# Performance work log

Hardware: AMD Instinct MI355X
Metric: run time of the kernel (lower is better)

The kernel has to match this reference:

```python
import jax, jax.numpy as jnp
import numpy as np

N_NODES = 100000


def _gcn_conv(x, row, col, W, b, n):
    # PyG GCNConv: h = W x; out_i = sum_{j->i} norm_ij * h_j + b, with self-loops
    # and symmetric normalization norm_ij = deg_i^-1/2 * deg_j^-1/2.
    h = x @ W  # [N, out]
    loop = jnp.arange(n, dtype=row.dtype)
    r = jnp.concatenate([row, loop])
    c = jnp.concatenate([col, loop])
    deg = jax.ops.segment_sum(jnp.ones_like(c, dtype=h.dtype), c, num_segments=n)
    dinv = jnp.where(deg > 0, jax.lax.rsqrt(deg), 0.0)
    norm = dinv[r] * dinv[c]  # [E+N]
    msg = h[r] * norm[:, None]  # gather + per-edge scale
    out = jax.ops.segment_sum(msg, c, num_segments=n)  # scatter-add to dst
    return out + b


def setup_inputs() -> dict:
    key = jax.random.key(0)
    ks = jax.random.split(key, 8)
    N, E = N_NODES, 1600000
    d_in, comm_dim, hid, out = 120, 8, 128, 64
    x = jax.random.normal(ks[0], (N, d_in), dtype=jnp.float32)
    edge_index = jax.random.randint(ks[1], (2, E), 0, N, dtype=jnp.int64)
    comm_ids = jax.random.randint(ks[2], (N,), 0, 64, dtype=jnp.int64)
    comm_emb = jax.random.normal(ks[3], (64, comm_dim), dtype=jnp.float32)
    s1 = 1.0 / np.sqrt(d_in + comm_dim)
    s2 = 1.0 / np.sqrt(hid)
    W1 = jax.random.normal(ks[4], (d_in + comm_dim, hid), dtype=jnp.float32) * s1
    b1 = jnp.zeros((hid,), dtype=jnp.float32)
    W2 = jax.random.normal(ks[5], (hid, out), dtype=jnp.float32) * s2
    b2 = jnp.zeros((out,), dtype=jnp.float32)
    return {"x": x, "edge_index": edge_index, "comm_ids": comm_ids,
            "comm_emb": comm_emb, "W1": W1, "b1": b1, "W2": W2, "b2": b2}


def reference(x, edge_index, comm_ids, comm_emb, W1, b1, W2, b2):
    n = x.shape[0]
    row, col = edge_index[0], edge_index[1]
    c = comm_emb[comm_ids]                      # [N, comm_dim] embedding lookup
    h = jnp.concatenate([x, c], axis=-1)        # [N, in+comm_dim]
    h = jax.nn.relu(_gcn_conv(h, row, col, W1, b1, n))
    # dropout p=0.5 is inactive in eval mode (training=False)
    out = _gcn_conv(h, row, col, W2, b2, n)     # [N, out_channels]
    return out
```

## Files before the change

kernel.cpp:

```cpp
#include <hip/hip_runtime.h>

typedef __attribute__((ext_vector_type(8))) short bf16x8;
typedef __attribute__((ext_vector_type(4))) float f32x4;

#define CAPB 5632
#define NBMAX 512

static __device__ __forceinline__ unsigned short f2bf(float f) {
    unsigned u = __float_as_uint(f);
    unsigned r = (u + 0x7fff + ((u >> 16) & 1)) >> 16;
    return (unsigned short)r;
}
static __device__ __forceinline__ float bfu_lo(unsigned v) { return __uint_as_float(v << 16); }
static __device__ __forceinline__ float bfu_hi(unsigned v) { return __uint_as_float(v & 0xffff0000u); }
static __device__ __forceinline__ unsigned packbf(float a, float b) {
    return (unsigned)f2bf(a) | ((unsigned)f2bf(b) << 16);
}

static __device__ __forceinline__ bf16x8 cvt8(float4 u0, float4 u1) {
    bf16x8 r;
    r[0] = (short)f2bf(u0.x); r[1] = (short)f2bf(u0.y);
    r[2] = (short)f2bf(u0.z); r[3] = (short)f2bf(u0.w);
    r[4] = (short)f2bf(u1.x); r[5] = (short)f2bf(u1.y);
    r[6] = (short)f2bf(u1.z); r[7] = (short)f2bf(u1.w);
    return r;
}

__global__ void k_zero_int(int* __restrict__ p, int n) {
    int i = blockIdx.x * blockDim.x + threadIdx.x;
    if (i < n) p[i] = 0;
}

__global__ __launch_bounds__(256) void k_passA(const int* __restrict__ row,
                                               const int* __restrict__ col,
                                               int* __restrict__ gcnt,
                                               unsigned* __restrict__ packed,
                                               int E, int NB) {
    __shared__ int lcnt[NBMAX];
    __shared__ int lbase[NBMAX];
    __shared__ int lcur[NBMAX];
    __shared__ int gbaseS[NBMAX];
    __shared__ unsigned stage[4096];
    __shared__ unsigned short stageb[4096];
    __shared__ int s[256];

    int tid = threadIdx.x;
    int t0 = blockIdx.x * 4096;
    int total = min(4096, E - t0);

    for (int b = tid; b < NBMAX; b += 256) { lcnt[b] = 0; lcur[b] = 0; }
    __syncthreads();

    int er[16], ec[16];
#pragma unroll
    for (int j = 0; j < 16; ++j) {
        int e = t0 + j * 256 + tid;
        if (e < E) {
            er[j] = row[e];
            ec[j] = col[e];
            atomicAdd(&lcnt[ec[j] >> 8], 1);
        }
    }
    __syncthreads();

    int c0 = lcnt[2 * tid], c1 = lcnt[2 * tid + 1];
    int p = c0 + c1;
    s[tid] = p;
    __syncthreads();
    for (int off = 1; off < 256; off <<= 1) {
        int t = (tid >= off) ? s[tid - off] : 0;
        __syncthreads();
        s[tid] += t;
        __syncthreads();
    }
    int ebase = s[tid] - p;
    lbase[2 * tid] = ebase;
    lbase[2 * tid + 1] = ebase + c0;
    __syncthreads();

    for (int b = tid; b < NB; b += 256) {
        int lc = lcnt[b];
        if (lc > 0) gbaseS[b] = atomicAdd(&gcnt[b], lc);
    }
    __syncthreads();

#pragma unroll
    for (int j = 0; j < 16; ++j) {
        int e = t0 + j * 256 + tid;
        if (e < E) {
            int b = ec[j] >> 8;
            int pos = lbase[b] + atomicAdd(&lcur[b], 1);
            stage[pos] = ((unsigned)er[j] << 8) | ((unsigned)ec[j] & 255u);
            stageb[pos] = (unsigned short)b;
        }
    }
    __syncthreads();

    for (int j = tid; j < total; j += 256) {
        int b = stageb[j];
        packed[(size_t)b * CAPB + gbaseS[b] + (j - lbase[b])] = stage[j];
    }
}

__global__ void k_bscan(const int* __restrict__ gcnt, int* __restrict__ gbase,
                        int* __restrict__ indptr, int n, int E, int NB) {
    __shared__ int s[512];
    int tid = threadIdx.x;
    int v = (tid < NB) ? gcnt[tid] : 0;
    s[tid] = v;
    __syncthreads();
    for (int off = 1; off < 512; off <<= 1) {
        int t = (tid >= off) ? s[tid - off] : 0;
        __syncthreads();
        s[tid] += t;
        __syncthreads();
    }
    if (tid < NB) gbase[tid] = s[tid] - v;
    if (tid == 0) indptr[n] = E;
}

__global__ __launch_bounds__(256) void k_passB(const unsigned* __restrict__ packed,
                                               const int* __restrict__ gcnt,
                                               const int* __restrict__ gbase,
                                               int* __restrict__ indptr,
                                               float* __restrict__ dinv,
                                               int* __restrict__ srcidx, int n) {
    __shared__ int ncnt[256];
    __shared__ int nbase[256];
    __shared__ int srow[CAPB];

    int b = blockIdx.x;
    int tid = threadIdx.x;
    int nodeBase = b << 8;
    int cntE = min(gcnt[b], CAPB);
    int base = gbase[b];
    size_t pb = (size_t)b * CAPB;

    ncnt[tid] = 0;
    __syncthreads();

    for (int j = tid; j < cntE; j += 256) {
        unsigned e = packed[pb + j];
        atomicAdd(&ncnt[e & 255u], 1);
    }
    __syncthreads();

    int v = ncnt[tid];
    nbase[tid] = v;
    __syncthreads();
    for (int off = 1; off < 256; off <<= 1) {
        int t = (tid >= off) ? nbase[tid - off] : 0;
        __syncthreads();
        nbase[tid] += t;
        __syncthreads();
    }
    int excl = nbase[tid] - v;
    __syncthreads();
    nbase[tid] = excl;

    int node = nodeBase + tid;
    if (node < n) {
        indptr[node] = base + excl;
        dinv[node] = rsqrtf((float)(v + 1));
    }
    ncnt[tid] = 0;
    __syncthreads();

    for (int j = tid; j < cntE; j += 256) {
        unsigned e = packed[pb + j];
        int c = (int)(e & 255u);
        int r = (int)(e >> 8);
        int p = nbase[c] + atomicAdd(&ncnt[c], 1);
        srow[p] = r;
    }
    __syncthreads();

    for (int j = tid; j < cntE; j += 256) srcidx[base + j] = srow[j];
}

__global__ void k_wprep(const float* __restrict__ W1, const float* __restrict__ W2,
                        unsigned short* __restrict__ Wt1, unsigned short* __restrict__ Wt2p) {
    int idx = blockIdx.x * blockDim.x + threadIdx.x;
    if (idx < 128 * 128) {
        int colc = idx >> 7, k = idx & 127;
        Wt1[colc * 128 + k] = f2bf(W1[k * 128 + colc]);
    } else if (idx < 128 * 128 + 64 * 128) {
        int j = idx - 128 * 128;
        int colc = j >> 7, p = j & 127;
        int korig = (p & 7) * 16 + (p >> 3);
        Wt2p[colc * 128 + p] = f2bf(W2[korig * 64 + colc]);
    }
}

__global__ __launch_bounds__(256) void k_gemm1(const float* __restrict__ x,
                                               const int* __restrict__ cid,
                                               const float* __restrict__ cemb,
                                               const unsigned short* __restrict__ Wt,
                                               const float* __restrict__ dinv,
                                               unsigned char* __restrict__ D1q,
                                               float* __restrict__ scales, int n) {
    int tid = threadIdx.x;
    int wid = tid >> 6, lane = tid & 63;
    int rbase = blockIdx.x * 64 + wid * 16;
    int lr = lane & 15, kq = lane >> 4;

    int arow = rbase + lr;
    if (arow > n - 1) arow = n - 1;
    const float* xp = x + (size_t)arow * 120 + kq * 8;

    bf16x8 a0 = cvt8(*(const float4*)(xp),      *(const float4*)(xp + 4));
    bf16x8 a1 = cvt8(*(const float4*)(xp + 32), *(const float4*)(xp + 36));
    bf16x8 a2 = cvt8(*(const float4*)(xp + 64), *(const float4*)(xp + 68));
    bf16x8 a3;
    if (kq < 3) {
        a3 = cvt8(*(const float4*)(xp + 96), *(const float4*)(xp + 100));
    } else {
        const float* cp = cemb + (size_t)cid[arow] * 8;
        a3 = cvt8(*(const float4*)(cp), *(const float4*)(cp + 4));
    }

    f32x4 acc[8];
#pragma unroll
    for (int cf = 0; cf < 8; ++cf) acc[cf] = (f32x4){0.f, 0.f, 0.f, 0.f};

#pragma unroll
    for (int cf = 0; cf < 8; ++cf) {
        const unsigned short* bp = Wt + (size_t)(cf * 16 + lr) * 128 + kq * 8;
        bf16x8 b0 = *(const bf16x8*)(bp);
        bf16x8 b1 = *(const bf16x8*)(bp + 32);
        bf16x8 b2 = *(const bf16x8*)(bp + 64);
        bf16x8 b3 = *(const bf16x8*)(bp + 96);
        acc[cf] = __builtin_amdgcn_mfma_f32_16x16x32_bf16(a0, b0, acc[cf], 0, 0, 0);
        acc[cf] = __builtin_amdgcn_mfma_f32_16x16x32_bf16(a1, b1, acc[cf], 0, 0, 0);
        acc[cf] = __builtin_amdgcn_mfma_f32_16x16x32_bf16(a2, b2, acc[cf], 0, 0, 0);
        acc[cf] = __builtin_amdgcn_mfma_f32_16x16x32_bf16(a3, b3, acc[cf], 0, 0, 0);
    }

#pragma unroll
    for (int r = 0; r < 4; ++r) {
        int grow = rbase + kq * 4 + r;
        float dv = (grow < n) ? dinv[grow] : 0.f;
        float m = 0.f;
#pragma unroll
        for (int cf = 0; cf < 8; ++cf) m = fmaxf(m, fabsf(acc[cf][r] * dv));
        m = fmaxf(m, __shfl_xor(m, 1));
        m = fmaxf(m, __shfl_xor(m, 2));
        m = fmaxf(m, __shfl_xor(m, 4));
        m = fmaxf(m, __shfl_xor(m, 8));
        float sinv = (m > 1e-20f) ? 127.f / m : 0.f;
        if (grow < n) {
            if (lr == 0) scales[grow] = m * (1.f / 127.f);
            unsigned lo = 0, hi = 0;
#pragma unroll
            for (int cf = 0; cf < 4; ++cf) {
                int q8 = (int)rintf(acc[cf][r] * dv * sinv);
                lo |= ((unsigned)(q8 & 255)) << (8 * cf);
            }
#pragma unroll
            for (int cf = 4; cf < 8; ++cf) {
                int q8 = (int)rintf(acc[cf][r] * dv * sinv);
                hi |= ((unsigned)(q8 & 255)) << (8 * (cf - 4));
            }
            *(uint2*)&D1q[(size_t)grow * 128 + lr * 8] = make_uint2(lo, hi);
        }
    }
}

template <int NOUT>
__global__ __launch_bounds__(256) void k_gemm_bf16(const unsigned short* __restrict__ A,
                                                   const unsigned short* __restrict__ Wt,
                                                   const float* __restrict__ dinv,
                                                   unsigned short* __restrict__ D, int n) {
    constexpr int NCF = NOUT / 16;
    int tid = threadIdx.x;
    int wid = tid >> 6, lane = tid & 63;
    int rbase = blockIdx.x * 64 + wid * 16;
    int lr = lane & 15, kq = lane >> 4;

    int arow = rbase + lr;
    if (arow > n - 1) arow = n - 1;
    const unsigned short* ap = A + (size_t)arow * 128 + kq * 8;
    bf16x8 a0 = *(const bf16x8*)(ap);
    bf16x8 a1 = *(const bf16x8*)(ap + 32);
    bf16x8 a2 = *(const bf16x8*)(ap + 64);
    bf16x8 a3 = *(const bf16x8*)(ap + 96);

    f32x4 acc[NCF];
#pragma unroll
    for (int cf = 0; cf < NCF; ++cf) acc[cf] = (f32x4){0.f, 0.f, 0.f, 0.f};

#pragma unroll
    for (int cf = 0; cf < NCF; ++cf) {
        const unsigned short* bp = Wt + (size_t)(cf * 16 + lr) * 128 + kq * 8;
        bf16x8 b0 = *(const bf16x8*)(bp);
        bf16x8 b1 = *(const bf16x8*)(bp + 32);
        bf16x8 b2 = *(const bf16x8*)(bp + 64);
        bf16x8 b3 = *(const bf16x8*)(bp + 96);
        acc[cf] = __builtin_amdgcn_mfma_f32_16x16x32_bf16(a0, b0, acc[cf], 0, 0, 0);
        acc[cf] = __builtin_amdgcn_mfma_f32_16x16x32_bf16(a1, b1, acc[cf], 0, 0, 0);
        acc[cf] = __builtin_amdgcn_mfma_f32_16x16x32_bf16(a2, b2, acc[cf], 0, 0, 0);
        acc[cf] = __builtin_amdgcn_mfma_f32_16x16x32_bf16(a3, b3, acc[cf], 0, 0, 0);
    }

    float dv[4];
#pragma unroll
    for (int r = 0; r < 4; ++r) {
        int grow = rbase + kq * 4 + r;
        dv[r] = (grow < n) ? dinv[grow] : 0.f;
    }
#pragma unroll
    for (int cf = 0; cf < NCF; ++cf) {
#pragma unroll
        for (int r = 0; r < 4; ++r) {
            int grow = rbase + kq * 4 + r;
            if (grow < n) D[(size_t)grow * NOUT + cf * 16 + lr] = f2bf(acc[cf][r] * dv[r]);
        }
    }
}

__global__ __launch_bounds__(64) void k_agg1(const unsigned char* __restrict__ Hq,
                                             const float* __restrict__ scales,
                                             const int* __restrict__ indptr,
                                             const int* __restrict__ srcidx,
                                             const float* __restrict__ dinv,
                                             const float* __restrict__ bias,
                                             unsigned* __restrict__ Out, int n) {
    int i = blockIdx.x;
    int lane = threadIdx.x;
    int c0 = ((2 * lane) & 7) * 16 + (lane >> 2);
    float bx = bias[c0], by = bias[c0 + 16];
    float di = dinv[i];

    unsigned short sq = *(const unsigned short*)(Hq + (size_t)i * 128 + 2 * lane);
    float ss = scales[i];
    float ax = ss * (float)(signed char)(sq & 255);
    float ay = ss * (float)(signed char)(sq >> 8);

    int e0 = indptr[i], e1 = indptr[i + 1];
#pragma unroll 4
    for (int e = e0; e < e1; ++e) {
        int s = srcidx[e];
        unsigned short q = *(const unsigned short*)(Hq + (size_t)s * 128 + 2 * lane);
        float sc = scales[s];
        ax += sc * (float)(signed char)(q & 255);
        ay += sc * (float)(signed char)(q >> 8);
    }
    float ox = fmaxf(di * ax + bx, 0.f);
    float oy = fmaxf(di * ay + by, 0.f);
    Out[(size_t)i * 64 + lane] = packbf(ox, oy);
}

__global__ __launch_bounds__(64) void k_agg2(const unsigned* __restrict__ Hs,
                                             const int* __restrict__ indptr,
                                             const int* __restrict__ srcidx,
                                             const float* __restrict__ dinv,
                                             const float* __restrict__ bias,
                                             float2* __restrict__ Out, int n) {
    int i = blockIdx.x;
    int lane = threadIdx.x;
    int v = lane & 31, h = lane >> 5;
    float di = dinv[i];
    float2 b = *(const float2*)&bias[v * 2];
    float ax = 0.f, ay = 0.f;
    if (h == 0) {
        unsigned sv = Hs[(size_t)i * 32 + v];
        ax = bfu_lo(sv);
        ay = bfu_hi(sv);
    }
    int e0 = indptr[i], e1 = indptr[i + 1];
#pragma unroll 4
    for (int e = e0 + h; e < e1; e += 2) {
        unsigned w = Hs[(size_t)srcidx[e] * 32 + v];
        ax += bfu_lo(w);
        ay += bfu_hi(w);
    }
    ax += __shfl_xor(ax, 32);
    ay += __shfl_xor(ay, 32);
    if (h == 0) {
        Out[(size_t)i * 32 + v] = make_float2(di * ax + b.x, di * ay + b.y);
    }
}


extern "C" void kernel_launch(void* const* d_in, const int* in_sizes, int n_in,
                              void* d_out, int out_size, void* d_ws, size_t ws_size,
                              hipStream_t stream) {
    const float* x    = (const float*)d_in[0];
    const int*   eidx = (const int*)d_in[1];
    const int*   cid  = (const int*)d_in[2];
    const float* cemb = (const float*)d_in[3];
    const float* W1   = (const float*)d_in[4];
    const float* b1   = (const float*)d_in[5];
    const float* W2   = (const float*)d_in[6];
    const float* b2   = (const float*)d_in[7];
    float* out = (float*)d_out;

    int n = in_sizes[2];
    int E = in_sizes[1] / 2;
    const int* row = eidx;
    const int* col = eidx + E;
    int NB = (n + 255) / 256;

    char* ws = (char*)d_ws;
    auto alloc = [&](size_t bytes) {
        char* p = ws;
        ws += (bytes + 255) & ~(size_t)255;
        return p;
    };
    float*          dinv   = (float*)alloc((size_t)n * 4);
    int*            gcnt   = (int*)alloc((size_t)NB * 4);
    int*            gbase  = (int*)alloc((size_t)NB * 4);
    int*            indptr = (int*)alloc((size_t)(n + 1) * 4);
    int*            srcidx = (int*)alloc((size_t)E * 4);
    unsigned*       packed = (unsigned*)alloc((size_t)NB * CAPB * 4);
    unsigned short* Wt1    = (unsigned short*)alloc(128 * 128 * 2);
    unsigned short* Wt2p   = (unsigned short*)alloc(64 * 128 * 2);
    unsigned char*  D1q    = (unsigned char*)alloc((size_t)n * 128);
    float*          scales = (float*)alloc((size_t)n * 4);
    unsigned short* H1p    = (unsigned short*)alloc((size_t)n * 128 * 2);
    unsigned short* D2     = (unsigned short*)alloc((size_t)n * 64 * 2);

    k_zero_int<<<(NB + 255) / 256, 256, 0, stream>>>(gcnt, NB);
    k_passA<<<(E + 4095) / 4096, 256, 0, stream>>>(row, col, gcnt, packed, E, NB);
    k_bscan<<<1, 512, 0, stream>>>(gcnt, gbase, indptr, n, E, NB);
    k_passB<<<NB, 256, 0, stream>>>(packed, gcnt, gbase, indptr, dinv, srcidx, n);

    k_wprep<<<(128 * 128 + 64 * 128 + 255) / 256, 256, 0, stream>>>(W1, W2, Wt1, Wt2p);

    int gb = (n + 63) / 64;
    k_gemm1<<<gb, 256, 0, stream>>>(x, cid, cemb, Wt1, dinv, D1q, scales, n);
    k_agg1<<<n, 64, 0, stream>>>(D1q, scales, indptr, srcidx, dinv, b1,
                                 (unsigned*)H1p, n);
    k_gemm_bf16<64><<<gb, 256, 0, stream>>>(H1p, Wt2p, dinv, D2, n);
    k_agg2<<<n, 64, 0, stream>>>((const unsigned*)D2, indptr, srcidx, dinv, b2,
                                 (float2*)out, n);
}
```

Baseline: 213.2 us.

## Pack four nodes per wavefront in aggregation kernels with wider per-lane loads

Both aggregation kernels now map four destination nodes onto each 64-lane wavefront, 16 lanes per node, instead of one node per block. Each lane loads 8 bytes per neighbor row (8 int8 or 4 bf16 values) rather than 2 or 4, and writes 16-byte outputs. To keep the column permutation consistent with the new per-lane mapping, bias b1 is permuted once in the weight-prep kernel. The goal is to cut block count and per-node launch and scheduling overhead and to issue fewer, wider memory requests. The cost is that the four nodes in a wave iterate to the largest degree among them, with masked dummy loads for the shorter ones.

```diff
diff --git a/kernel.cpp b/kernel.cpp
--- a/kernel.cpp
+++ b/kernel.cpp
@@ -179,7 +179,9 @@
 }
 
 __global__ void k_wprep(const float* __restrict__ W1, const float* __restrict__ W2,
-                        unsigned short* __restrict__ Wt1, unsigned short* __restrict__ Wt2p) {
+                        const float* __restrict__ b1,
+                        unsigned short* __restrict__ Wt1, unsigned short* __restrict__ Wt2p,
+                        float* __restrict__ b1p) {
     int idx = blockIdx.x * blockDim.x + threadIdx.x;
     if (idx < 128 * 128) {
         int colc = idx >> 7, k = idx & 127;
@@ -189,6 +191,9 @@
         int colc = j >> 7, p = j & 127;
         int korig = (p & 7) * 16 + (p >> 3);
         Wt2p[colc * 128 + p] = f2bf(W2[korig * 64 + colc]);
+    } else if (idx < 128 * 128 + 64 * 128 + 128) {
+        int p = idx - (128 * 128 + 64 * 128);
+        b1p[p] = b1[(p & 7) * 16 + (p >> 3)];
     }
 }
 
@@ -318,67 +323,93 @@
     }
 }
 
-__global__ __launch_bounds__(64) void k_agg1(const unsigned char* __restrict__ Hq,
+__global__ __launch_bounds__(64) void k_agg1(const uint2* __restrict__ rows,
                                              const float* __restrict__ scales,
                                              const int* __restrict__ indptr,
                                              const int* __restrict__ srcidx,
                                              const float* __restrict__ dinv,
-                                             const float* __restrict__ bias,
-                                             unsigned* __restrict__ Out, int n) {
-    int i = blockIdx.x;
+                                             const float* __restrict__ b1p,
+                                             uint4* __restrict__ Out, int n) {
     int lane = threadIdx.x;
-    int c0 = ((2 * lane) & 7) * 16 + (lane >> 2);
-    float bx = bias[c0], by = bias[c0 + 16];
+    int g = lane >> 4, gl = lane & 15;
+    int i = blockIdx.x * 4 + g;
+    if (i > n - 1) i = n - 1;
+
     float di = dinv[i];
-
-    unsigned short sq = *(const unsigned short*)(Hq + (size_t)i * 128 + 2 * lane);
+    float4 bA = *(const float4*)&b1p[gl * 8];
+    float4 bB = *(const float4*)&b1p[gl * 8 + 4];
+
+    uint2 sq = rows[(size_t)i * 16 + gl];
     float ss = scales[i];
-    float ax = ss * (float)(signed char)(sq & 255);
-    float ay = ss * (float)(signed char)(sq >> 8);
-
-    int e0 = indptr[i], e1 = indptr[i + 1];
+    float a[8];
+#pragma unroll
+    for (int j = 0; j < 4; ++j) {
+        a[j]     = ss * (float)(signed char)((sq.x >> (8 * j)) & 255u);
+        a[j + 4] = ss * (float)(signed char)((sq.y >> (8 * j)) & 255u);
+    }
+
+    int e0 = indptr[i];
+    int d = indptr[i + 1] - e0;
+    int m = max(d, __shfl_xor(d, 16));
+    m = max(m, __shfl_xor(m, 32));
+
 #pragma unroll 4
-    for (int e = e0; e < e1; ++e) {
-        int s = srcidx[e];
-        unsigned short q = *(const unsigned short*)(Hq + (size_t)s * 128 + 2 * lane);
-        float sc = scales[s];
-        ax += sc * (float)(signed char)(q & 255);
-        ay += sc * (float)(signed char)(q >> 8);
-    }
-    float ox = fmaxf(di * ax + bx, 0.f);
-    float oy = fmaxf(di * ay + by, 0.f);
-    Out[(size_t)i * 64 + lane] = packbf(ox, oy);
-}
-
-__global__ __launch_bounds__(64) void k_agg2(const unsigned* __restrict__ Hs,
+    for (int t = 0; t < m; ++t) {
+        bool act = t < d;
+        int s = act ? srcidx[e0 + t] : i;
+        float sc = act ? scales[s] : 0.f;
+        uint2 q = rows[(size_t)s * 16 + gl];
+#pragma unroll
+        for (int j = 0; j < 4; ++j) {
+            a[j]     += sc * (float)(signed char)((q.x >> (8 * j)) & 255u);
+            a[j + 4] += sc * (float)(signed char)((q.y >> (8 * j)) & 255u);
+        }
+    }
+
+    uint4 o;
+    o.x = packbf(fmaxf(di * a[0] + bA.x, 0.f), fmaxf(di * a[1] + bA.y, 0.f));
+    o.y = packbf(fmaxf(di * a[2] + bA.z, 0.f), fmaxf(di * a[3] + bA.w, 0.f));
+    o.z = packbf(fmaxf(di * a[4] + bB.x, 0.f), fmaxf(di * a[5] + bB.y, 0.f));
+    o.w = packbf(fmaxf(di * a[6] + bB.z, 0.f), fmaxf(di * a[7] + bB.w, 0.f));
+    Out[(size_t)i * 16 + gl] = o;
+}
+
+__global__ __launch_bounds__(64) void k_agg2(const uint2* __restrict__ Hs,
                                              const int* __restrict__ indptr,
                                              const int* __restrict__ srcidx,
                                              const float* __restrict__ dinv,
                                              const float* __restrict__ bias,
-                                             float2* __restrict__ Out, int n) {
-    int i = blockIdx.x;
+                                             float4* __restrict__ Out, int n) {
     int lane = threadIdx.x;
-    int v = lane & 31, h = lane >> 5;
+    int g = lane >> 4, gl = lane & 15;
+    int i = blockIdx.x * 4 + g;
+    if (i > n - 1) i = n - 1;
+
     float di = dinv[i];
-    float2 b = *(const float2*)&bias[v * 2];
-    float ax = 0.f, ay = 0.f;
-    if (h == 0) {
-        unsigned sv = Hs[(size_t)i * 32 + v];
-        ax = bfu_lo(sv);
-        ay = bfu_hi(sv);
-    }
-    int e0 = indptr[i], e1 = indptr[i + 1];
+    float4 b = *(const float4*)&bias[gl * 4];
+
+    uint2 sv = Hs[(size_t)i * 16 + gl];
+    float a0 = bfu_lo(sv.x), a1 = bfu_hi(sv.x);
+    float a2 = bfu_lo(sv.y), a3 = bfu_hi(sv.y);
+
+    int e0 = indptr[i];
+    int d = indptr[i + 1] - e0;
+    int m = max(d, __shfl_xor(d, 16));
+    m = max(m, __shfl_xor(m, 32));
+
 #pragma unroll 4
-    for (int e = e0 + h; e < e1; e += 2) {
-        unsigned w = Hs[(size_t)srcidx[e] * 32 + v];
-        ax += bfu_lo(w);
-        ay += bfu_hi(w);
-    }
-    ax += __shfl_xor(ax, 32);
-    ay += __shfl_xor(ay, 32);
-    if (h == 0) {
-        Out[(size_t)i * 32 + v] = make_float2(di * ax + b.x, di * ay + b.y);
-    }
+    for (int t = 0; t < m; ++t) {
+        bool act = t < d;
+        int s = act ? srcidx[e0 + t] : i;
+        float msk = act ? 1.f : 0.f;
+        uint2 w = Hs[(size_t)s * 16 + gl];
+        a0 += msk * bfu_lo(w.x);
+        a1 += msk * bfu_hi(w.x);
+        a2 += msk * bfu_lo(w.y);
+        a3 += msk * bfu_hi(w.y);
+    }
+    Out[(size_t)i * 16 + gl] = make_float4(di * a0 + b.x, di * a1 + b.y,
+                                           di * a2 + b.z, di * a3 + b.w);
 }
 
 
@@ -415,6 +446,7 @@
     unsigned*       packed = (unsigned*)alloc((size_t)NB * CAPB * 4);
     unsigned short* Wt1    = (unsigned short*)alloc(128 * 128 * 2);
     unsigned short* Wt2p   = (unsigned short*)alloc(64 * 128 * 2);
+    float*          b1p    = (float*)alloc(128 * 4);
     unsigned char*  D1q    = (unsigned char*)alloc((size_t)n * 128);
     float*          scales = (float*)alloc((size_t)n * 4);
     unsigned short* H1p    = (unsigned short*)alloc((size_t)n * 128 * 2);
@@ -425,13 +457,15 @@
     k_bscan<<<1, 512, 0, stream>>>(gcnt, gbase, indptr, n, E, NB);
     k_passB<<<NB, 256, 0, stream>>>(packed, gcnt, gbase, indptr, dinv, srcidx, n);
 
-    k_wprep<<<(128 * 128 + 64 * 128 + 255) / 256, 256, 0, stream>>>(W1, W2, Wt1, Wt2p);
+    k_wprep<<<(128 * 128 + 64 * 128 + 128 + 255) / 256, 256, 0, stream>>>(W1, W2, b1,
+                                                                          Wt1, Wt2p, b1p);
 
     int gb = (n + 63) / 64;
+    int ga = (n + 3) / 4;
     k_gemm1<<<gb, 256, 0, stream>>>(x, cid, cemb, Wt1, dinv, D1q, scales, n);
-    k_agg1<<<n, 64, 0, stream>>>(D1q, scales, indptr, srcidx, dinv, b1,
-                                 (unsigned*)H1p, n);
+    k_agg1<<<ga, 64, 0, stream>>>((const uint2*)D1q, scales, indptr, srcidx, dinv, b1p,
+                                  (uint4*)H1p, n);
     k_gemm_bf16<64><<<gb, 256, 0, stream>>>(H1p, Wt2p, dinv, D2, n);
-    k_agg2<<<n, 64, 0, stream>>>((const unsigned*)D2, indptr, srcidx, dinv, b2,
-                                 (float2*)out, n);
-}
+    k_agg2<<<ga, 64, 0, stream>>>((const uint2*)D2, indptr, srcidx, dinv, b2,
+                                  (float4*)out, n);
+}
```

Result: faster. 195.2 us (-8.5%).
